# Performance work log

Measured on AMD Instinct MI355X. Metric: run time of the kernel, lower is better.

## Reference

```python
import jax, jax.numpy as jnp
import numpy as np

B, T, S, D = 64, 512, 512, 256


def setup_inputs() -> dict:
    key = jax.random.key(0)
    ks = jax.random.split(key, 8)
    s = 1.0 / np.sqrt(D)  # pytorch LSTM init scale
    return {
        "decoder_embeds": jax.random.normal(ks[0], (B, T, D), jnp.float32),
        "h0": jax.random.normal(ks[1], (1, B, D), jnp.float32),
        "c0": jax.random.normal(ks[2], (1, B, D), jnp.float32),
        "encoder_output": jax.random.normal(ks[3], (B, S, D), jnp.float32),
        "W_ih": jax.random.uniform(ks[4], (4 * D, D), jnp.float32, -s, s),
        "W_hh": jax.random.uniform(ks[5], (4 * D, D), jnp.float32, -s, s),
        "b_ih": jax.random.uniform(ks[6], (4 * D,), jnp.float32, -s, s),
        "b_hh": jax.random.uniform(ks[7], (4 * D,), jnp.float32, -s, s),
    }


def _lstm_outputs(decoder_embeds, h0, c0, W_ih, W_hh, b_ih, b_hh):
    # Faithful to source: step 0 input is decoder_embeds[:,0]; afterwards the
    # previous LSTM OUTPUT is fed back (decoder_embeds[:,1:] are unused).
    d = decoder_embeds.shape[-1]
    bias = b_ih + b_hh  # [4D]

    def step(carry, _):
        x, h, c = carry  # each [B, D]
        gates = x @ W_ih.T + h @ W_hh.T + bias  # [B, 4D]
        i, f, g, o = jnp.split(gates, 4, axis=-1)  # pytorch gate order i,f,g,o
        c_new = jax.nn.sigmoid(f) * c + jax.nn.sigmoid(i) * jnp.tanh(g)
        h_new = jax.nn.sigmoid(o) * jnp.tanh(c_new)
        return (h_new, h_new, c_new), h_new

    init = (decoder_embeds[:, 0, :], h0[0], c0[0])
    _, H = jax.lax.scan(step, init, None, length=decoder_embeds.shape[1])
    return jnp.transpose(H, (1, 0, 2))  # [B, T, D]


def reference(decoder_embeds, h0, c0, encoder_output, W_ih, W_hh, b_ih, b_hh):
    H = _lstm_outputs(decoder_embeds, h0, c0, W_ih, W_hh, b_ih, b_hh)  # [B,T,D]
    # use_attention=True: per-step bmm attention; h_t only depends on the scan,
    # so attention is computed vectorized over T (same math).
    scores = jnp.einsum("btd,bsd->bts", H, encoder_output)  # [B,T,S]
    attn = jax.nn.softmax(scores, axis=-1)
    ctx = jnp.einsum("bts,bsd->btd", attn, encoder_output)  # [B,T,D]
    return jnp.concatenate([H, ctx], axis=-1)  # [B,T,2D]
```

## Files before the change

kernel.cpp:

```cpp
#include <hip/hip_runtime.h>
#include <cstdint>
#include <cstddef>

#define B_  64
#define T_  512
#define S_  512
#define D_  256

#define GROUPS 16
#define BPG    16

typedef __attribute__((ext_vector_type(4))) float f32x4;
typedef __attribute__((ext_vector_type(8))) short bf16x8;

union UBF { bf16x8 v; uint32_t u[4]; };
union USH { bf16x8 v; ushort s[8]; };

__device__ __forceinline__ ushort f2bf(float f) {
    union { float f; uint32_t u; } v; v.f = f;
    uint32_t r = v.u + 0x7FFFu + ((v.u >> 16) & 1u);
    return (ushort)(r >> 16);
}
__device__ __forceinline__ float bf2f(ushort h) {
    union { uint32_t u; float f; } v; v.u = ((uint32_t)h) << 16; return v.f;
}
__device__ __forceinline__ uint4 ldx4u_cg(const uint32_t* p) {
    uint4 r;
    asm volatile("global_load_dwordx4 %0, %1, off sc0 sc1\n\ts_waitcnt vmcnt(0)"
                 : "=v"(r) : "v"(p) : "memory");
    return r;
}
__device__ __forceinline__ void st_cg_u32(uint32_t* p, uint32_t v) {
    asm volatile("global_store_dword %0, %1, off sc0 sc1" :: "v"(p), "v"(v) : "memory");
}
__device__ __forceinline__ uint32_t hi2(uint32_t a, uint32_t b) {
#if __has_builtin(__builtin_amdgcn_perm)
    return __builtin_amdgcn_perm(b, a, 0x07060302u);
#else
    return (a >> 16) | (b & 0xFFFF0000u);
#endif
}

__global__ __launch_bounds__(256) void ws_init(uint32_t* __restrict__ hbuf) {
    int i = blockIdx.x * 256 + threadIdx.x;
    if (i < 2 * 16384)
        __hip_atomic_store(hbuf + i, 0xFFFFFFFFu, __ATOMIC_RELAXED, __HIP_MEMORY_SCOPE_AGENT);
}


__global__ __launch_bounds__(256, 1) void lstm_persistent(
    const float* __restrict__ de,  const float* __restrict__ h0,
    const float* __restrict__ c0,
    const float* __restrict__ Wih, const float* __restrict__ Whh,
    const float* __restrict__ bih, const float* __restrict__ bhh,
    float* __restrict__ out, uint32_t* __restrict__ hbuf)
{
    __shared__ uint32_t hlds[4 * 260];
    __shared__ float    glds[256];
    __shared__ float    t0buf[2][4][256];

    const int tid = threadIdx.x;
    const int grp = blockIdx.x >> 4;
    const int jb  = blockIdx.x & 15;

    const int w  = tid >> 6;
    const int l  = tid & 63;
    const int lr = l & 15;
    const int lg = l >> 4;

    const int cb  = tid & 3;
    const int cd  = tid >> 2;
    const int bx  = grp * 4 + cb;
    const int dxc = jb * 16 + cd;

    float c_reg = 0.f;
    float bsum0 = 0.f, bsum1 = 0.f, bsum2 = 0.f, bsum3 = 0.f;
    if (tid < 64) {
        c_reg = c0[(size_t)bx * 256 + dxc];
        bsum0 = bih[      jb * 16 + cd] + bhh[      jb * 16 + cd];
        bsum1 = bih[256 + jb * 16 + cd] + bhh[256 + jb * 16 + cd];
        bsum2 = bih[512 + jb * 16 + cd] + bhh[512 + jb * 16 + cd];
        bsum3 = bih[768 + jb * 16 + cd] + bhh[768 + jb * 16 + cd];
    }

    bf16x8 Ahi[8], Alo[8];

    #pragma unroll
    for (int m = 0; m < 8; ++m) {
        int idx = m * 256 + tid;
        int arr = idx >> 10, bl = (idx >> 8) & 3, k = idx & 255;
        t0buf[arr][bl][k] = arr ? h0[(size_t)(grp * 4 + bl) * 256 + k]
                                : de[(size_t)(grp * 4 + bl) * T_ * D_ + k];
    }
    __syncthreads();
    {
        int r = tid >> 2, bq = tid & 3;
        int gr = (r >> 4) * 256 + jb * 16 + (r & 15);
        const float4* wi4 = (const float4*)(Wih + (size_t)gr * 256);
        const float4* wh4 = (const float4*)(Whh + (size_t)gr * 256);
        const float4* e4  = (const float4*)(&t0buf[0][bq][0]);
        const float4* h4  = (const float4*)(&t0buf[1][bq][0]);
        float a0 = 0.f, a1 = 0.f, a2 = 0.f, a3 = 0.f;
        #pragma unroll 8
        for (int k4 = 0; k4 < 64; ++k4) {
            float4 x = wi4[k4], y = e4[k4];
            a0 += x.x*y.x; a1 += x.y*y.y; a2 += x.z*y.z; a3 += x.w*y.w;
            x = wh4[k4]; y = h4[k4];
            a0 += x.x*y.x; a1 += x.y*y.y; a2 += x.z*y.z; a3 += x.w*y.w;
        }
        glds[(r >> 4) * 64 + (r & 15) * 4 + bq] = (a0 + a1) + (a2 + a3);
    }

    for (int t = 0; t < T_; ++t) {
        if (t > 0) {
            const uint32_t expc = (uint32_t)(t - 1);
            const uint32_t* hp = hbuf + ((t - 1) & 1) * 16384 + grp * 1024 + tid * 4;
            uint4 v = ldx4u_cg(hp);
            while ((((v.x ^ expc) | (v.y ^ expc) | (v.z ^ expc) | (v.w ^ expc)) & 0xFFFFu) != 0u)
                v = ldx4u_cg(hp);
            *(uint4*)(hlds + (tid >> 6) * 260 + (tid & 63) * 4) = v;
            __syncthreads();

            f32x4 acch = (f32x4){0.f, 0.f, 0.f, 0.f};
            f32x4 accl = (f32x4){0.f, 0.f, 0.f, 0.f};
            const uint32_t* hrow = hlds + (lr & 3) * 260 + lg * 8;
            #pragma unroll
            for (int kt = 0; kt < 8; ++kt) {
                uint4 q0 = *(const uint4*)(hrow + kt * 32);
                uint4 q1 = *(const uint4*)(hrow + kt * 32 + 4);
                UBF bb;
                bb.u[0] = hi2(q0.x, q0.y);
                bb.u[1] = hi2(q0.z, q0.w);
                bb.u[2] = hi2(q1.x, q1.y);
                bb.u[3] = hi2(q1.z, q1.w);
                acch = __builtin_amdgcn_mfma_f32_16x16x32_bf16(Ahi[kt], bb.v, acch, 0, 0, 0);
                accl = __builtin_amdgcn_mfma_f32_16x16x32_bf16(Alo[kt], bb.v, accl, 0, 0, 0);
            }
            f32x4 acc = acch + accl;
            if (lr < 4) {
                glds[w * 64 + (lg * 4 + 0) * 4 + lr] = acc[0];
                glds[w * 64 + (lg * 4 + 1) * 4 + lr] = acc[1];
                glds[w * 64 + (lg * 4 + 2) * 4 + lr] = acc[2];
                glds[w * 64 + (lg * 4 + 3) * 4 + lr] = acc[3];
            }
        }
        __syncthreads();

        if (tid < 64) {
            float gi = glds[      cd * 4 + cb] + bsum0;
            float gf = glds[ 64 + cd * 4 + cb] + bsum1;
            float gg = glds[128 + cd * 4 + cb] + bsum2;
            float go = glds[192 + cd * 4 + cb] + bsum3;
            float si = 1.f / (1.f + __expf(-gi));
            float sf = 1.f / (1.f + __expf(-gf));
            float so = 1.f / (1.f + __expf(-go));
            float tg = 1.f - 2.f / (1.f + __expf(2.f * gg));
            c_reg = sf * c_reg + si * tg;
            float tc = 1.f - 2.f / (1.f + __expf(2.f * c_reg));
            float hn = so * tc;
            if (t < T_ - 1) {
                uint32_t pk = ((uint32_t)f2bf(hn) << 16) | (uint32_t)t;
                st_cg_u32(hbuf + (t & 1) * 16384 + grp * 1024 + cb * 256 + dxc, pk);
            }
            out[((size_t)bx * T_ + t) * 512 + dxc] = hn;
        }

        if (t == 0) {
            int gr = w * 256 + jb * 16 + lr;
            const float4* wi4 = (const float4*)(Wih + (size_t)gr * 256);
            const float4* wh4 = (const float4*)(Whh + (size_t)gr * 256);
            #pragma unroll
            for (int kt = 0; kt < 8; ++kt) {
                float4 p  = wi4[kt * 8 + lg * 2], q  = wi4[kt * 8 + lg * 2 + 1];
                float4 r4 = wh4[kt * 8 + lg * 2], s4 = wh4[kt * 8 + lg * 2 + 1];
                float f[8] = {p.x + r4.x, p.y + r4.y, p.z + r4.z, p.w + r4.w,
                              q.x + s4.x, q.y + s4.y, q.z + s4.z, q.w + s4.w};
                USH hi, lo;
                #pragma unroll
                for (int j = 0; j < 8; ++j) {
                    ushort h = f2bf(f[j]);
                    hi.s[j] = h;
                    lo.s[j] = f2bf(f[j] - bf2f(h));
                }
                Ahi[kt] = hi.v; Alo[kt] = lo.v;
            }
        }
    }
}


__global__ __launch_bounds__(256, 2) void attn_kernel(
    const float* __restrict__ E, float* __restrict__ out)
{
    __shared__ alignas(16) ushort Ech [32 * 264];
    __shared__ alignas(16) ushort EchT[256 * 40];
    __shared__ alignas(16) ushort Phi[4][16 * 40];
    __shared__ alignas(16) ushort Plo[4][16 * 40];

    const int id  = blockIdx.x;
    const int xcd = id & 7, rr = id >> 3;
    const int tt  = rr & 7,  bh = rr >> 3;
    const int b   = bh * 8 + xcd;
    const int t0  = tt * 64;

    const int tid = threadIdx.x;
    const int w   = tid >> 6;
    const int l   = tid & 63;
    const int lr  = l & 15;
    const int lg  = l >> 4;

    bf16x8 Ahi[8], Alo[8];
    {
        const float* Hrow = out + ((size_t)b * T_ + (t0 + w * 16 + lr)) * 512;
        #pragma unroll
        for (int kt = 0; kt < 8; ++kt) {
            float4 x0 = *(const float4*)(Hrow + kt * 32 + lg * 8);
            float4 x1 = *(const float4*)(Hrow + kt * 32 + lg * 8 + 4);
            float f[8] = {x0.x, x0.y, x0.z, x0.w, x1.x, x1.y, x1.z, x1.w};
            USH hi, lo;
            #pragma unroll
            for (int j = 0; j < 8; ++j) {
                ushort h = f2bf(f[j]);
                hi.s[j] = h;
                lo.s[j] = f2bf(f[j] - bf2f(h));
            }
            Ahi[kt] = hi.v; Alo[kt] = lo.v;
        }
    }

    f32x4 ctx[16];
    #pragma unroll
    for (int i = 0; i < 16; ++i) ctx[i] = (f32x4){0.f, 0.f, 0.f, 0.f};
    float mrow[4] = {-1e30f, -1e30f, -1e30f, -1e30f};
    float srow[4] = {0.f, 0.f, 0.f, 0.f};

    const float* Eb = E + (size_t)b * S_ * 256;

    for (int c = 0; c < 16; ++c) {
        #pragma unroll
        for (int m = 0; m < 8; ++m) {
            int idx = m * 256 + tid;
            int sr = idx >> 6, k4 = idx & 63;
            float4 e = *(const float4*)(Eb + (size_t)(c * 32 + sr) * 256 + 4 * k4);
            ushort4 u;
            u.x = f2bf(e.x); u.y = f2bf(e.y); u.z = f2bf(e.z); u.w = f2bf(e.w);
            *(ushort4*)(&Ech[sr * 264 + 4 * k4]) = u;
        }
        __syncthreads();

        f32x4 sacc0 = (f32x4){0.f,0.f,0.f,0.f};
        f32x4 sacc1 = (f32x4){0.f,0.f,0.f,0.f};
        #pragma unroll
        for (int kt = 0; kt < 8; ++kt) {
            bf16x8 Bf0 = *(const bf16x8*)(&Ech[(0 * 16 + lr) * 264 + kt * 32 + lg * 8]);
            bf16x8 Bf1 = *(const bf16x8*)(&Ech[(1 * 16 + lr) * 264 + kt * 32 + lg * 8]);
            sacc0 = __builtin_amdgcn_mfma_f32_16x16x32_bf16(Ahi[kt], Bf0, sacc0, 0, 0, 0);
            sacc0 = __builtin_amdgcn_mfma_f32_16x16x32_bf16(Alo[kt], Bf0, sacc0, 0, 0, 0);
            sacc1 = __builtin_amdgcn_mfma_f32_16x16x32_bf16(Ahi[kt], Bf1, sacc1, 0, 0, 0);
            sacc1 = __builtin_amdgcn_mfma_f32_16x16x32_bf16(Alo[kt], Bf1, sacc1, 0, 0, 0);
        }

        #pragma unroll
        for (int m = 0; m < 8; ++m) {
            int idx = m * 256 + tid;
            int s = idx & 31, kq = idx >> 5;
            ushort4 v = *(const ushort4*)(&Ech[s * 264 + 4 * kq]);
            EchT[(4 * kq + 0) * 40 + s] = v.x;
            EchT[(4 * kq + 1) * 40 + s] = v.y;
            EchT[(4 * kq + 2) * 40 + s] = v.z;
            EchT[(4 * kq + 3) * 40 + s] = v.w;
        }

        float cmax[4], p0[4], p1[4], csum[4], mnew[4], scale[4];
        #pragma unroll
        for (int g = 0; g < 4; ++g) cmax[g] = fmaxf(sacc0[g], sacc1[g]);
        #pragma unroll
        for (int d = 1; d < 16; d <<= 1) {
            #pragma unroll
            for (int g = 0; g < 4; ++g) cmax[g] = fmaxf(cmax[g], __shfl_xor(cmax[g], d));
        }
        #pragma unroll
        for (int g = 0; g < 4; ++g) {
            mnew[g]  = fmaxf(mrow[g], cmax[g]);
            scale[g] = __expf(mrow[g] - mnew[g]);
            p0[g] = __expf(sacc0[g] - mnew[g]);
            p1[g] = __expf(sacc1[g] - mnew[g]);
            csum[g] = p0[g] + p1[g];
        }
        #pragma unroll
        for (int d = 1; d < 16; d <<= 1) {
            #pragma unroll
            for (int g = 0; g < 4; ++g) csum[g] += __shfl_xor(csum[g], d);
        }
        #pragma unroll
        for (int g = 0; g < 4; ++g) {
            srow[g] = srow[g] * scale[g] + csum[g];
            mrow[g] = mnew[g];
        }
        #pragma unroll
        for (int i = 0; i < 16; ++i) {
            ctx[i][0] *= scale[0]; ctx[i][1] *= scale[1];
            ctx[i][2] *= scale[2]; ctx[i][3] *= scale[3];
        }
        #pragma unroll
        for (int g = 0; g < 4; ++g) {
            int rrw = (lg * 4 + g) * 40;
            ushort h0v = f2bf(p0[g]);
            Phi[w][rrw + lr]      = h0v;
            Plo[w][rrw + lr]      = f2bf(p0[g] - bf2f(h0v));
            ushort h1v = f2bf(p1[g]);
            Phi[w][rrw + 16 + lr] = h1v;
            Plo[w][rrw + 16 + lr] = f2bf(p1[g] - bf2f(h1v));
        }
        __syncthreads();

        {
            bf16x8 Ap = *(const bf16x8*)(&Phi[w][lr * 40 + lg * 8]);
            bf16x8 Aq = *(const bf16x8*)(&Plo[w][lr * 40 + lg * 8]);
            #pragma unroll
            for (int dt = 0; dt < 16; ++dt) {
                bf16x8 Bf = *(const bf16x8*)(&EchT[(dt * 16 + lr) * 40 + lg * 8]);
                ctx[dt] = __builtin_amdgcn_mfma_f32_16x16x32_bf16(Ap, Bf, ctx[dt], 0, 0, 0);
                ctx[dt] = __builtin_amdgcn_mfma_f32_16x16x32_bf16(Aq, Bf, ctx[dt], 0, 0, 0);
            }
        }
        __syncthreads();
    }

    float inv[4];
    #pragma unroll
    for (int g = 0; g < 4; ++g) inv[g] = 1.f / srow[g];
    #pragma unroll
    for (int dt = 0; dt < 16; ++dt) {
        #pragma unroll
        for (int g = 0; g < 4; ++g) {
            out[((size_t)b * T_ + (t0 + w * 16 + lg * 4 + g)) * 512 + 256 + dt * 16 + lr] =
                ctx[dt][g] * inv[g];
        }
    }
}


extern "C" void kernel_launch(void* const* d_in, const int* in_sizes, int n_in,
                              void* d_out, int out_size, void* d_ws, size_t ws_size,
                              hipStream_t stream)
{
    const float* de  = (const float*)d_in[0];
    const float* h0  = (const float*)d_in[1];
    const float* c0  = (const float*)d_in[2];
    const float* E   = (const float*)d_in[3];
    const float* Wih = (const float*)d_in[4];
    const float* Whh = (const float*)d_in[5];
    const float* bih = (const float*)d_in[6];
    const float* bhh = (const float*)d_in[7];
    float* out  = (float*)d_out;
    uint32_t* hbuf = (uint32_t*)d_ws;

    ws_init<<<128, 256, 0, stream>>>(hbuf);

    void* args[] = {(void*)&de, (void*)&h0, (void*)&c0, (void*)&Wih, (void*)&Whh,
                    (void*)&bih, (void*)&bhh, (void*)&out, (void*)&hbuf};
    hipLaunchCooperativeKernel((const void*)lstm_persistent,
                               dim3(GROUPS * BPG), dim3(256), args, 0, stream);

    attn_kernel<<<dim3(512), 256, 0, stream>>>(E, out);
}
```

Baseline: 1.019 ms.

## Reorder MFMA weight rows so gates land in registers, skip LDS gate exchange

Weight rows are permuted so each lane's MFMA accumulator holds all four gates (i,f,g,o) for one (batch, hidden) pair. The elementwise LSTM update then runs straight from registers in every wave, not via an LDS round-trip followed by a second barrier and a single-wave tail. The t=0 step is peeled out of the loop, which removes the per-step branches. The goal is to shorten the serial per-timestep critical path of the recurrence. The cost is redundant gate math in the lanes that do not store, plus a barrier at the end of each step to protect the hlds reuse.

Result: faster. 965.2 us (-5.3%).

```diff
diff --git a/kernel.cpp b/kernel.cpp
--- a/kernel.cpp
+++ b/kernel.cpp
@@ -68,29 +68,25 @@
     const int lr = l & 15;
     const int lg = l >> 4;
 
-    const int cb  = tid & 3;
-    const int cd  = tid >> 2;
-    const int bx  = grp * 4 + cb;
-    const int dxc = jb * 16 + cd;
-
-    float c_reg = 0.f;
-    float bsum0 = 0.f, bsum1 = 0.f, bsum2 = 0.f, bsum3 = 0.f;
-    if (tid < 64) {
-        c_reg = c0[(size_t)bx * 256 + dxc];
-        bsum0 = bih[      jb * 16 + cd] + bhh[      jb * 16 + cd];
-        bsum1 = bih[256 + jb * 16 + cd] + bhh[256 + jb * 16 + cd];
-        bsum2 = bih[512 + jb * 16 + cd] + bhh[512 + jb * 16 + cd];
-        bsum3 = bih[768 + jb * 16 + cd] + bhh[768 + jb * 16 + cd];
-    }
+    const int bl = lr & 3;
+    const int bx = grp * 4 + bl;
+    const int dx = jb * 16 + w * 4 + lg;
+    const bool store_lane = (lr < 4);
+
+    const float bs0 = bih[      dx] + bhh[      dx];
+    const float bs1 = bih[256 + dx] + bhh[256 + dx];
+    const float bs2 = bih[512 + dx] + bhh[512 + dx];
+    const float bs3 = bih[768 + dx] + bhh[768 + dx];
+    float c_reg = c0[(size_t)bx * 256 + dx];
 
     bf16x8 Ahi[8], Alo[8];
 
     #pragma unroll
     for (int m = 0; m < 8; ++m) {
         int idx = m * 256 + tid;
-        int arr = idx >> 10, bl = (idx >> 8) & 3, k = idx & 255;
-        t0buf[arr][bl][k] = arr ? h0[(size_t)(grp * 4 + bl) * 256 + k]
-                                : de[(size_t)(grp * 4 + bl) * T_ * D_ + k];
+        int arr = idx >> 10, bq = (idx >> 8) & 3, k = idx & 255;
+        t0buf[arr][bq][k] = arr ? h0[(size_t)(grp * 4 + bq) * 256 + k]
+                                : de[(size_t)(grp * 4 + bq) * T_ * D_ + k];
     }
     __syncthreads();
     {
@@ -110,47 +106,80 @@
         }
         glds[(r >> 4) * 64 + (r & 15) * 4 + bq] = (a0 + a1) + (a2 + a3);
     }
-
-    for (int t = 0; t < T_; ++t) {
-        if (t > 0) {
-            const uint32_t expc = (uint32_t)(t - 1);
-            const uint32_t* hp = hbuf + ((t - 1) & 1) * 16384 + grp * 1024 + tid * 4;
-            uint4 v = ldx4u_cg(hp);
-            while ((((v.x ^ expc) | (v.y ^ expc) | (v.z ^ expc) | (v.w ^ expc)) & 0xFFFFu) != 0u)
-                v = ldx4u_cg(hp);
-            *(uint4*)(hlds + (tid >> 6) * 260 + (tid & 63) * 4) = v;
-            __syncthreads();
-
-            f32x4 acch = (f32x4){0.f, 0.f, 0.f, 0.f};
-            f32x4 accl = (f32x4){0.f, 0.f, 0.f, 0.f};
-            const uint32_t* hrow = hlds + (lr & 3) * 260 + lg * 8;
-            #pragma unroll
-            for (int kt = 0; kt < 8; ++kt) {
-                uint4 q0 = *(const uint4*)(hrow + kt * 32);
-                uint4 q1 = *(const uint4*)(hrow + kt * 32 + 4);
-                UBF bb;
-                bb.u[0] = hi2(q0.x, q0.y);
-                bb.u[1] = hi2(q0.z, q0.w);
-                bb.u[2] = hi2(q1.x, q1.y);
-                bb.u[3] = hi2(q1.z, q1.w);
-                acch = __builtin_amdgcn_mfma_f32_16x16x32_bf16(Ahi[kt], bb.v, acch, 0, 0, 0);
-                accl = __builtin_amdgcn_mfma_f32_16x16x32_bf16(Alo[kt], bb.v, accl, 0, 0, 0);
+    __syncthreads();
+
+    {
+        int d16 = w * 4 + lg;
+        float gi = glds[      d16 * 4 + bl] + bs0;
+        float gf = glds[ 64 + d16 * 4 + bl] + bs1;
+        float gg = glds[128 + d16 * 4 + bl] + bs2;
+        float go = glds[192 + d16 * 4 + bl] + bs3;
+        float si = 1.f / (1.f + __expf(-gi));
+        float sf = 1.f / (1.f + __expf(-gf));
+        float so = 1.f / (1.f + __expf(-go));
+        float tg = 1.f - 2.f / (1.f + __expf(2.f * gg));
+        c_reg = sf * c_reg + si * tg;
+        float tc = 1.f - 2.f / (1.f + __expf(2.f * c_reg));
+        float hn = so * tc;
+        if (store_lane) {
+            uint32_t pk = ((uint32_t)f2bf(hn) << 16);
+            st_cg_u32(hbuf + 0 * 16384 + grp * 1024 + bl * 256 + dx, pk);
+            out[((size_t)bx * T_ + 0) * 512 + dx] = hn;
+        }
+    }
+
+    {
+        int gr = (lr & 3) * 256 + jb * 16 + w * 4 + (lr >> 2);
+        const float4* wi4 = (const float4*)(Wih + (size_t)gr * 256);
+        const float4* wh4 = (const float4*)(Whh + (size_t)gr * 256);
+        #pragma unroll
+        for (int kt = 0; kt < 8; ++kt) {
+            float4 p  = wi4[kt * 8 + lg * 2], q  = wi4[kt * 8 + lg * 2 + 1];
+            float4 r4 = wh4[kt * 8 + lg * 2], s4 = wh4[kt * 8 + lg * 2 + 1];
+            float f[8] = {p.x + r4.x, p.y + r4.y, p.z + r4.z, p.w + r4.w,
+                          q.x + s4.x, q.y + s4.y, q.z + s4.z, q.w + s4.w};
+            USH hi, lo;
+            #pragma unroll
+            for (int j = 0; j < 8; ++j) {
+                ushort h = f2bf(f[j]);
+                hi.s[j] = h;
+                lo.s[j] = f2bf(f[j] - bf2f(h));
             }
-            f32x4 acc = acch + accl;
-            if (lr < 4) {
-                glds[w * 64 + (lg * 4 + 0) * 4 + lr] = acc[0];
-                glds[w * 64 + (lg * 4 + 1) * 4 + lr] = acc[1];
-                glds[w * 64 + (lg * 4 + 2) * 4 + lr] = acc[2];
-                glds[w * 64 + (lg * 4 + 3) * 4 + lr] = acc[3];
-            }
-        }
-        __syncthreads();
-
-        if (tid < 64) {
-            float gi = glds[      cd * 4 + cb] + bsum0;
-            float gf = glds[ 64 + cd * 4 + cb] + bsum1;
-            float gg = glds[128 + cd * 4 + cb] + bsum2;
-            float go = glds[192 + cd * 4 + cb] + bsum3;
+            Ahi[kt] = hi.v; Alo[kt] = lo.v;
+        }
+    }
+
+    for (int t = 1; t < T_; ++t) {
+        const uint32_t expc = (uint32_t)(t - 1);
+        const uint32_t* hp = hbuf + ((t - 1) & 1) * 16384 + grp * 1024 + tid * 4;
+        uint4 v = ldx4u_cg(hp);
+        while ((((v.x ^ expc) | (v.y ^ expc) | (v.z ^ expc) | (v.w ^ expc)) & 0xFFFFu) != 0u)
+            v = ldx4u_cg(hp);
+        *(uint4*)(hlds + (tid >> 6) * 260 + (tid & 63) * 4) = v;
+        __syncthreads();
+
+        f32x4 acch = (f32x4){0.f, 0.f, 0.f, 0.f};
+        f32x4 accl = (f32x4){0.f, 0.f, 0.f, 0.f};
+        const uint32_t* hrow = hlds + (lr & 3) * 260 + lg * 8;
+        #pragma unroll
+        for (int kt = 0; kt < 8; ++kt) {
+            uint4 q0 = *(const uint4*)(hrow + kt * 32);
+            uint4 q1 = *(const uint4*)(hrow + kt * 32 + 4);
+            UBF bb;
+            bb.u[0] = hi2(q0.x, q0.y);
+            bb.u[1] = hi2(q0.z, q0.w);
+            bb.u[2] = hi2(q1.x, q1.y);
+            bb.u[3] = hi2(q1.z, q1.w);
+            acch = __builtin_amdgcn_mfma_f32_16x16x32_bf16(Ahi[kt], bb.v, acch, 0, 0, 0);
+            accl = __builtin_amdgcn_mfma_f32_16x16x32_bf16(Alo[kt], bb.v, accl, 0, 0, 0);
+        }
+        f32x4 acc = acch + accl;
+
+        {
+            float gi = acc[0] + bs0;
+            float gf = acc[1] + bs1;
+            float gg = acc[2] + bs2;
+            float go = acc[3] + bs3;
             float si = 1.f / (1.f + __expf(-gi));
             float sf = 1.f / (1.f + __expf(-gf));
             float so = 1.f / (1.f + __expf(-go));
@@ -158,33 +187,15 @@
             c_reg = sf * c_reg + si * tg;
             float tc = 1.f - 2.f / (1.f + __expf(2.f * c_reg));
             float hn = so * tc;
-            if (t < T_ - 1) {
-                uint32_t pk = ((uint32_t)f2bf(hn) << 16) | (uint32_t)t;
-                st_cg_u32(hbuf + (t & 1) * 16384 + grp * 1024 + cb * 256 + dxc, pk);
+            if (store_lane) {
+                if (t < T_ - 1) {
+                    uint32_t pk = ((uint32_t)f2bf(hn) << 16) | (uint32_t)t;
+                    st_cg_u32(hbuf + (t & 1) * 16384 + grp * 1024 + bl * 256 + dx, pk);
+                }
+                out[((size_t)bx * T_ + t) * 512 + dx] = hn;
             }
-            out[((size_t)bx * T_ + t) * 512 + dxc] = hn;
-        }
-
-        if (t == 0) {
-            int gr = w * 256 + jb * 16 + lr;
-            const float4* wi4 = (const float4*)(Wih + (size_t)gr * 256);
-            const float4* wh4 = (const float4*)(Whh + (size_t)gr * 256);
-            #pragma unroll
-            for (int kt = 0; kt < 8; ++kt) {
-                float4 p  = wi4[kt * 8 + lg * 2], q  = wi4[kt * 8 + lg * 2 + 1];
-                float4 r4 = wh4[kt * 8 + lg * 2], s4 = wh4[kt * 8 + lg * 2 + 1];
-                float f[8] = {p.x + r4.x, p.y + r4.y, p.z + r4.z, p.w + r4.w,
-                              q.x + s4.x, q.y + s4.y, q.z + s4.z, q.w + s4.w};
-                USH hi, lo;
-                #pragma unroll
-                for (int j = 0; j < 8; ++j) {
-                    ushort h = f2bf(f[j]);
-                    hi.s[j] = h;
-                    lo.s[j] = f2bf(f[j] - bf2f(h));
-                }
-                Ahi[kt] = hi.v; Alo[kt] = lo.v;
-            }
-        }
+        }
+        __syncthreads();
     }
 }
 
```
